# Kernel tuning notes

Hardware: AMD Instinct MI355X
Metric: run time of the kernel (lower is better)

## Reference

```python
import jax, jax.numpy as jnp
import numpy as np

NUM_FORMULAS = 1024
INPUT_DIM = 256
BATCH = 2048


def setup_inputs() -> dict:
    key = jax.random.key(0)
    k_x, k_mu, k_sigma = jax.random.split(key, 3)
    inputs = jax.random.normal(k_x, (BATCH, INPUT_DIM), dtype=jnp.float32)
    # keras random_normal initializer default stddev = 0.05
    mu = 0.05 * jax.random.normal(k_mu, (NUM_FORMULAS, INPUT_DIM), dtype=jnp.float32)
    sigma = 0.05 * jax.random.normal(k_sigma, (1, NUM_FORMULAS, INPUT_DIM), dtype=jnp.float32)
    temperature = jnp.float32(2.0)
    return {"inputs": inputs, "mu": mu, "sigma": sigma, "temperature": temperature}


def reference(inputs, mu, sigma, temperature):
    # diff: (batch, num_formulas, dim)
    diff = inputs[:, None, :] - mu[None, :, :]
    # weighted L2 norm over feature dim -> (batch, num_formulas)
    dist = jnp.sqrt(jnp.sum(jnp.square(diff * sigma), axis=-1))
    loc = jnp.exp(-dist)
    # sigmoid-gated temperature, softmax over formulas (last axis)
    return jax.nn.softmax(jax.nn.sigmoid(temperature) * loc, axis=-1)
```

## Files before the change

### kernel.cpp

```cpp
#include <hip/hip_runtime.h>
#include <math.h>

#define NF 1024
#define DIM 256
#define BATCH 2048
#define K 512
#define BM 64
#define BN 64
#define KB 64
#define LDA 80
#define NCHUNK (NF / BN)

#define WS_B_BYTES  (NF * K * 2)
#define WS_C_OFF    WS_B_BYTES
#define WS_RP_OFF   (WS_B_BYTES + NF * 4)

typedef __attribute__((ext_vector_type(8))) short short8;
typedef __attribute__((ext_vector_type(4))) float f32x4;

__device__ inline unsigned short f2bf(float f) {
    unsigned u = __float_as_uint(f);
    u += 0x7fffu + ((u >> 16) & 1u);
    return (unsigned short)(u >> 16);
}

__global__ __launch_bounds__(256) void k_prep(const float* __restrict__ mu,
                                              const float* __restrict__ sigma,
                                              unsigned int* __restrict__ Bb32,
                                              float* __restrict__ c,
                                              float4* __restrict__ rowPartial4) {
    const int t = threadIdx.x;
    if (blockIdx.x >= NF) {
        const int zb = blockIdx.x - NF;
        rowPartial4[zb * 256 + t] = make_float4(0.f, 0.f, 0.f, 0.f);
        return;
    }
    const int f = blockIdx.x;
    const float m = mu[f * DIM + t];
    const float s = sigma[f * DIM + t];
    const float s2 = s * s;
    const float w = -2.0f * s2 * m;
    Bb32[f * DIM + t] = (unsigned)f2bf(s2) | ((unsigned)f2bf(w) << 16);

    float cp = s2 * m * m;
    #pragma unroll
    for (int off = 32; off > 0; off >>= 1) cp += __shfl_down(cp, off, 64);
    __shared__ float red[4];
    const int lane = t & 63, wv = t >> 6;
    if (lane == 0) red[wv] = cp;
    __syncthreads();
    if (t == 0) c[f] = red[0] + red[1] + red[2] + red[3];
}

__global__ __launch_bounds__(256, 2) void k_main(const float* __restrict__ x,
                                                 const ushort* __restrict__ Bb,
                                                 const float* __restrict__ c,
                                                 const float* __restrict__ temp,
                                                 float* __restrict__ out,
                                                 float* __restrict__ rowPartial) {
    const int t = threadIdx.x;
    const int w = t >> 6;
    const int lane = t & 63;
    const int m16 = lane & 15;
    const int q = lane >> 4;
    const int r0 = blockIdx.x * BM;
    const int n0 = blockIdx.y * BN;

    __shared__ ushort Alds[BM * LDA];
    __shared__ float sums[4][BM];

    f32x4 acc[4];
    #pragma unroll
    for (int rt = 0; rt < 4; ++rt) acc[rt] = (f32x4){0.f, 0.f, 0.f, 0.f};

    const float4* __restrict__ x4 = (const float4*)x;
    const int srow = t >> 3;
    const int dq = t & 7;

    const int fcol = n0 + w * 16 + m16;
    const ushort* __restrict__ Brow = Bb + fcol * K;

    for (int kb = 0; kb < K; kb += KB) {
        const int db4 = (kb >> 3);
        __syncthreads();
        #pragma unroll
        for (int h = 0; h < 2; ++h) {
            const int row = srow + h * 32;
            const float4 v = x4[(r0 + row) * (DIM / 4) + db4 + dq];
            short8 pk;
            pk[0] = (short)f2bf(v.x * v.x); pk[1] = (short)f2bf(v.x);
            pk[2] = (short)f2bf(v.y * v.y); pk[3] = (short)f2bf(v.y);
            pk[4] = (short)f2bf(v.z * v.z); pk[5] = (short)f2bf(v.z);
            pk[6] = (short)f2bf(v.w * v.w); pk[7] = (short)f2bf(v.w);
            *(short8*)&Alds[row * LDA + dq * 8] = pk;
        }
        __syncthreads();

        #pragma unroll
        for (int ks = 0; ks < KB; ks += 32) {
            const short8 bf = *(const short8*)&Brow[kb + ks + q * 8];
            #pragma unroll
            for (int rt = 0; rt < 4; ++rt) {
                const short8 af =
                    *(const short8*)&Alds[(rt * 16 + m16) * LDA + ks + q * 8];
                acc[rt] = __builtin_amdgcn_mfma_f32_16x16x32_bf16(af, bf, acc[rt], 0, 0, 0);
            }
        }
    }

    const float g = 1.0f / (1.0f + __expf(-temp[0]));
    const float cn = c[fcol];
    #pragma unroll
    for (int rt = 0; rt < 4; ++rt) {
        float s[4];
        #pragma unroll
        for (int i = 0; i < 4; ++i) {
            const float dist2 = acc[rt][i] + cn;
            const float dist = sqrtf(fmaxf(dist2, 0.0f));
            const float p = __expf(g * __expf(-dist));
            const int row = r0 + rt * 16 + q * 4 + i;
            out[row * NF + fcol] = p;
            s[i] = p;
        }
        #pragma unroll
        for (int i = 0; i < 4; ++i) {
            #pragma unroll
            for (int mask = 1; mask < 16; mask <<= 1)
                s[i] += __shfl_xor(s[i], mask, 64);
        }
        if (m16 == 0) {
            #pragma unroll
            for (int i = 0; i < 4; ++i) sums[w][rt * 16 + q * 4 + i] = s[i];
        }
    }
    __syncthreads();
    if (t < BM) {
        rowPartial[blockIdx.y * BATCH + r0 + t] =
            sums[0][t] + sums[1][t] + sums[2][t] + sums[3][t];
    }
}

__global__ __launch_bounds__(256) void k_norm(float* __restrict__ out,
                                              const float* __restrict__ rowPartial) {
    const int row = blockIdx.x;
    float ssum = 0.0f;
    #pragma unroll
    for (int ch = 0; ch < NCHUNK; ++ch) ssum += rowPartial[ch * BATCH + row];
    const float inv = 1.0f / ssum;
    float4* o4 = (float4*)(out + row * NF);
    float4 v = o4[threadIdx.x];
    v.x *= inv; v.y *= inv; v.z *= inv; v.w *= inv;
    o4[threadIdx.x] = v;
}

extern "C" void kernel_launch(void* const* d_in, const int* in_sizes, int n_in,
                              void* d_out, int out_size, void* d_ws, size_t ws_size,
                              hipStream_t stream) {
    const float* x     = (const float*)d_in[0];
    const float* mu    = (const float*)d_in[1];
    const float* sigma = (const float*)d_in[2];
    const float* temp  = (const float*)d_in[3];
    float* out = (float*)d_out;

    char* ws = (char*)d_ws;
    ushort* Bb        = (ushort*)ws;
    float*  c         = (float*)(ws + WS_C_OFF);
    float*  rowPartial = (float*)(ws + WS_RP_OFF);

    k_prep<<<NF + 32, 256, 0, stream>>>(mu, sigma, (unsigned int*)Bb, c,
                                        (float4*)rowPartial);

    dim3 g2(BATCH / BM, NF / BN);
    k_main<<<g2, 256, 0, stream>>>(x, Bb, c, temp, out, rowPartial);

    k_norm<<<BATCH, 256, 0, stream>>>(out, rowPartial);
}
```

Before: 83.39 us.

## Pre-convert inputs to bf16 and stage both GEMM operands in swizzled LDS

The bf16 packing of x and x^2 moves out of the main loop into the prep kernel, which now writes an A operand to workspace. The main kernel loads both A and B tiles straight into LDS with global_load_lds, using an XOR swizzle to avoid bank conflicts. Each wave now computes a 2x2 grid of MFMA tiles instead of 4x1, so each operand fragment is reused twice. This removes the repeated per-block conversion and the uncached per-lane B reads, at the cost of an extra A write/read pass through global memory. The rowPartial zeroing is dropped, which is safe because every entry is fully overwritten.

```diff
diff --git a/kernel.cpp b/kernel.cpp
--- a/kernel.cpp
+++ b/kernel.cpp
@@ -8,39 +8,46 @@
 #define BM 64
 #define BN 64
 #define KB 64
-#define LDA 80
 #define NCHUNK (NF / BN)
 
-#define WS_B_BYTES  (NF * K * 2)
-#define WS_C_OFF    WS_B_BYTES
-#define WS_RP_OFF   (WS_B_BYTES + NF * 4)
+#define WS_A_BYTES (BATCH * K * 2)
+#define WS_B_OFF   WS_A_BYTES
+#define WS_C_OFF   (WS_A_BYTES + NF * K * 2)
+#define WS_RP_OFF  (WS_C_OFF + NF * 4)
 
 typedef __attribute__((ext_vector_type(8))) short short8;
 typedef __attribute__((ext_vector_type(4))) float f32x4;
 
-__device__ inline unsigned short f2bf(float f) {
+__device__ __forceinline__ unsigned short f2bf(float f) {
     unsigned u = __float_as_uint(f);
     u += 0x7fffu + ((u >> 16) & 1u);
     return (unsigned short)(u >> 16);
 }
 
+__device__ __forceinline__ void gl_lds16(const ushort* g, ushort* l) {
+    __builtin_amdgcn_global_load_lds(
+        (const __attribute__((address_space(1))) void*)g,
+        (__attribute__((address_space(3))) void*)l, 16, 0, 0);
+}
+
 __global__ __launch_bounds__(256) void k_prep(const float* __restrict__ mu,
                                               const float* __restrict__ sigma,
+                                              const float* __restrict__ x,
+                                              unsigned int* __restrict__ Ab32,
                                               unsigned int* __restrict__ Bb32,
-                                              float* __restrict__ c,
-                                              float4* __restrict__ rowPartial4) {
+                                              float* __restrict__ c) {
     const int t = threadIdx.x;
     if (blockIdx.x >= NF) {
-        const int zb = blockIdx.x - NF;
-        rowPartial4[zb * 256 + t] = make_float4(0.f, 0.f, 0.f, 0.f);
+        const int i = (blockIdx.x - NF) * 256 + t;
+        const float v = x[i];
+        Ab32[i] = (unsigned)f2bf(v * v) | ((unsigned)f2bf(v) << 16);
         return;
     }
     const int f = blockIdx.x;
     const float m = mu[f * DIM + t];
     const float s = sigma[f * DIM + t];
     const float s2 = s * s;
-    const float w = -2.0f * s2 * m;
-    Bb32[f * DIM + t] = (unsigned)f2bf(s2) | ((unsigned)f2bf(w) << 16);
+    Bb32[f * DIM + t] = (unsigned)f2bf(s2) | ((unsigned)f2bf(-2.0f * s2 * m) << 16);
 
     float cp = s2 * m * m;
     #pragma unroll
@@ -52,7 +59,7 @@
     if (t == 0) c[f] = red[0] + red[1] + red[2] + red[3];
 }
 
-__global__ __launch_bounds__(256, 2) void k_main(const float* __restrict__ x,
+__global__ __launch_bounds__(256, 2) void k_main(const ushort* __restrict__ Ab,
                                                  const ushort* __restrict__ Bb,
                                                  const float* __restrict__ c,
                                                  const float* __restrict__ temp,
@@ -63,64 +70,74 @@
     const int lane = t & 63;
     const int m16 = lane & 15;
     const int q = lane >> 4;
+    const int wr = w >> 1, wc = w & 1;
     const int r0 = blockIdx.x * BM;
     const int n0 = blockIdx.y * BN;
 
-    __shared__ ushort Alds[BM * LDA];
-    __shared__ float sums[4][BM];
+    __shared__ __align__(16) ushort lds[8192];
+    __shared__ float sums[4][32];
 
-    f32x4 acc[4];
+    f32x4 acc[2][2];
     #pragma unroll
-    for (int rt = 0; rt < 4; ++rt) acc[rt] = (f32x4){0.f, 0.f, 0.f, 0.f};
+    for (int rt = 0; rt < 2; ++rt)
+        #pragma unroll
+        for (int ct = 0; ct < 2; ++ct) acc[rt][ct] = (f32x4){0.f, 0.f, 0.f, 0.f};
 
-    const float4* __restrict__ x4 = (const float4*)x;
-    const int srow = t >> 3;
-    const int dq = t & 7;
-
-    const int fcol = n0 + w * 16 + m16;
-    const ushort* __restrict__ Brow = Bb + fcol * K;
+    int srow[2], skc[2];
+    #pragma unroll
+    for (int h = 0; h < 2; ++h) {
+        const int s = h * 256 + t;
+        srow[h] = s >> 3;
+        skc[h] = (s & 7) ^ (srow[h] & 7);
+    }
 
     for (int kb = 0; kb < K; kb += KB) {
-        const int db4 = (kb >> 3);
         __syncthreads();
         #pragma unroll
         for (int h = 0; h < 2; ++h) {
-            const int row = srow + h * 32;
-            const float4 v = x4[(r0 + row) * (DIM / 4) + db4 + dq];
-            short8 pk;
-            pk[0] = (short)f2bf(v.x * v.x); pk[1] = (short)f2bf(v.x);
-            pk[2] = (short)f2bf(v.y * v.y); pk[3] = (short)f2bf(v.y);
-            pk[4] = (short)f2bf(v.z * v.z); pk[5] = (short)f2bf(v.z);
-            pk[6] = (short)f2bf(v.w * v.w); pk[7] = (short)f2bf(v.w);
-            *(short8*)&Alds[row * LDA + dq * 8] = pk;
+            const int s = h * 256 + t;
+            gl_lds16(Ab + (r0 + srow[h]) * K + kb + skc[h] * 8, &lds[s * 8]);
+            gl_lds16(Bb + (n0 + srow[h]) * K + kb + skc[h] * 8, &lds[4096 + s * 8]);
         }
         __syncthreads();
 
         #pragma unroll
         for (int ks = 0; ks < KB; ks += 32) {
-            const short8 bf = *(const short8*)&Brow[kb + ks + q * 8];
+            const int kcq = (ks >> 3) + q;
+            short8 av[2], bv[2];
             #pragma unroll
-            for (int rt = 0; rt < 4; ++rt) {
-                const short8 af =
-                    *(const short8*)&Alds[(rt * 16 + m16) * LDA + ks + q * 8];
-                acc[rt] = __builtin_amdgcn_mfma_f32_16x16x32_bf16(af, bf, acc[rt], 0, 0, 0);
+            for (int j = 0; j < 2; ++j) {
+                const int ar = wr * 32 + j * 16 + m16;
+                av[j] = *(const short8*)&lds[(ar * 8 + (kcq ^ (ar & 7))) * 8];
+                const int fr = wc * 32 + j * 16 + m16;
+                bv[j] = *(const short8*)&lds[4096 + (fr * 8 + (kcq ^ (fr & 7))) * 8];
             }
+            #pragma unroll
+            for (int rt = 0; rt < 2; ++rt)
+                #pragma unroll
+                for (int ct = 0; ct < 2; ++ct)
+                    acc[rt][ct] = __builtin_amdgcn_mfma_f32_16x16x32_bf16(
+                        av[rt], bv[ct], acc[rt][ct], 0, 0, 0);
         }
     }
 
     const float g = 1.0f / (1.0f + __expf(-temp[0]));
-    const float cn = c[fcol];
     #pragma unroll
-    for (int rt = 0; rt < 4; ++rt) {
-        float s[4];
+    for (int rt = 0; rt < 2; ++rt) {
+        float s[4] = {0.f, 0.f, 0.f, 0.f};
         #pragma unroll
-        for (int i = 0; i < 4; ++i) {
-            const float dist2 = acc[rt][i] + cn;
-            const float dist = sqrtf(fmaxf(dist2, 0.0f));
-            const float p = __expf(g * __expf(-dist));
-            const int row = r0 + rt * 16 + q * 4 + i;
-            out[row * NF + fcol] = p;
-            s[i] = p;
+        for (int ct = 0; ct < 2; ++ct) {
+            const int fcol = n0 + wc * 32 + ct * 16 + m16;
+            const float cn = c[fcol];
+            #pragma unroll
+            for (int i = 0; i < 4; ++i) {
+                const float dist2 = acc[rt][ct][i] + cn;
+                const float dist = sqrtf(fmaxf(dist2, 0.0f));
+                const float p = __expf(g * __expf(-dist));
+                const int row = r0 + wr * 32 + rt * 16 + q * 4 + i;
+                out[row * NF + fcol] = p;
+                s[i] += p;
+            }
         }
         #pragma unroll
         for (int i = 0; i < 4; ++i) {
@@ -135,8 +152,9 @@
     }
     __syncthreads();
     if (t < BM) {
+        const int half = t >> 5, lr = t & 31;
         rowPartial[blockIdx.y * BATCH + r0 + t] =
-            sums[0][t] + sums[1][t] + sums[2][t] + sums[3][t];
+            sums[half * 2][lr] + sums[half * 2 + 1][lr];
     }
 }
 
@@ -163,15 +181,17 @@
     float* out = (float*)d_out;
 
     char* ws = (char*)d_ws;
-    ushort* Bb        = (ushort*)ws;
+    ushort* Ab        = (ushort*)ws;
+    ushort* Bb        = (ushort*)(ws + WS_B_OFF);
     float*  c         = (float*)(ws + WS_C_OFF);
     float*  rowPartial = (float*)(ws + WS_RP_OFF);
 
-    k_prep<<<NF + 32, 256, 0, stream>>>(mu, sigma, (unsigned int*)Bb, c,
-                                        (float4*)rowPartial);
+    k_prep<<<NF + BATCH * DIM / 256, 256, 0, stream>>>(mu, sigma, x,
+                                                       (unsigned int*)Ab,
+                                                       (unsigned int*)Bb, c);
 
     dim3 g2(BATCH / BM, NF / BN);
-    k_main<<<g2, 256, 0, stream>>>(x, Bb, c, temp, out, rowPartial);
+    k_main<<<g2, 256, 0, stream>>>(Ab, Bb, c, temp, out, rowPartial);
 
     k_norm<<<BATCH, 256, 0, stream>>>(out, rowPartial);
 }
```

Measured after the change: 80.75 us. -3.2%, faster.
